# Kernel tuning notes

Measured on AMD Instinct MI355X. Metric: run time of the kernel, lower is better.

The kernel has to match this reference:

```python
import jax, jax.numpy as jnp
import numpy as np

DIMS = [1024, 2048, 2048, 51]
B, P = 16, 1024


def setup_inputs() -> dict:
    key = jax.random.key(0)
    ks = jax.random.split(key, 1 + 2 * (len(DIMS) - 1))
    inp = {
        "num_pairs": P,
        "classifier_input": jax.random.normal(ks[0], (B, P, DIMS[0]), dtype=jnp.float32),
        "num_batches": B,
    }
    # Linear params, PyTorch-style: W[out, in], b[out]
    for li in range(len(DIMS) - 1):
        fan_in = DIMS[li]
        bound = 1.0 / np.sqrt(fan_in)
        inp[f"W{li}"] = jax.random.uniform(ks[1 + 2 * li], (DIMS[li + 1], fan_in), minval=-bound, maxval=bound, dtype=jnp.float32)
        inp[f"b{li}"] = jax.random.uniform(ks[2 + 2 * li], (DIMS[li + 1],), minval=-bound, maxval=bound, dtype=jnp.float32)
    return inp


def reference(num_pairs, classifier_input, num_batches, W0, b0, W1, b1, W2, b2):
    # Batched MLP over all (num_batches * num_pairs) vectors at once.
    # Original loops per (b, i); math is identical. dropout p=0.0 -> identity.
    x = classifier_input  # [B, P, d_in]
    x = jax.nn.relu(jnp.einsum("bpd,hd->bph", x, W0) + b0)
    x = jax.nn.relu(jnp.einsum("bpd,hd->bph", x, W1) + b1)
    out = jnp.einsum("bpd,od->bpo", x, W2) + b2  # [B, P, n_classes]
    return out
```

## Files before the change

kernel.cpp:

```cpp
#include <hip/hip_runtime.h>
#include <hip/hip_bf16.h>
#include <stdint.h>

typedef __attribute__((ext_vector_type(8))) short short8;
typedef __attribute__((ext_vector_type(8))) uint16_t ushort8;
typedef __attribute__((ext_vector_type(4))) float floatx4;

#define TK 64


__device__ __forceinline__ uint16_t f2bf_bits(float f) {
    uint32_t u = __builtin_bit_cast(uint32_t, f);
    u += 0x7FFFu + ((u >> 16) & 1u);
    return (uint16_t)(u >> 16);
}

__device__ __forceinline__ void async_copy16(const void* g, void* l) {
    auto gp = (const __attribute__((address_space(1))) uint32_t*)(uintptr_t)g;
    auto lp = (__attribute__((address_space(3))) uint32_t*)(uint32_t)(uintptr_t)l;
    __builtin_amdgcn_global_load_lds(gp, lp, 16, 0, 0);
}

__device__ __forceinline__ void cvt8_one(const float* __restrict__ s, uint16_t* __restrict__ d) {
    floatx4 a = *(const floatx4*)(s);
    floatx4 b = *(const floatx4*)(s + 4);
    ushort8 o;
#pragma unroll
    for (int k = 0; k < 4; k++) { o[k] = f2bf_bits(a[k]); o[k + 4] = f2bf_bits(b[k]); }
    *(ushort8*)(d) = o;
}


__global__ void cvt8(const float* __restrict__ src, uint16_t* __restrict__ dst, int n) {
    int i = (blockIdx.x * 256 + threadIdx.x) * 8;
    if (i < n) cvt8_one(src + i, dst + i);
}

__global__ void cvt_weights(const float* __restrict__ W0, const float* __restrict__ W1,
                            const float* __restrict__ W2,
                            uint16_t* __restrict__ o0, uint16_t* __restrict__ o1,
                            uint16_t* __restrict__ o2) {
    int i = (blockIdx.x * 256 + threadIdx.x) * 8;
    if (i < 2097152) {
        cvt8_one(W0 + i, o0 + i);
    } else if (i < 2097152 + 4194304) {
        int j = i - 2097152;
        cvt8_one(W1 + j, o1 + j);
    } else {
        int j = i - 6291456;
        if (j < 131072) {
            int row = j >> 11;
            if (row < 51) cvt8_one(W2 + j, o2 + j);
            else { ushort8 z = {0,0,0,0,0,0,0,0}; *(ushort8*)(o2 + j) = z; }
        }
    }
}

__global__ void reduce_out(const float* __restrict__ part, const float* __restrict__ b2,
                           float* __restrict__ out, int M) {
    int idx = blockIdx.x * 256 + threadIdx.x;
    int o = idx & 63;
    if (o < 51) {
        int m = idx >> 6;
        float s = b2[o];
#pragma unroll
        for (int k = 0; k < 8; k++) s += part[(size_t)k * M * 64 + idx];
        out[m * 51 + o] = s;
    }
}


template <int MI, int NJ, int SPLITK, bool RELU, bool PARTIAL>
__global__ __launch_bounds__(256, 2)
void gemm_bt(const uint16_t* __restrict__ A,
             const uint16_t* __restrict__ W,
             const float* __restrict__ bias,
             void* __restrict__ out,
             int M, int N, int lda, int kspan, int ldc, int nstore)
{
    constexpr int TMv = MI * 32;
    constexpr int TNv = NJ * 32;
    constexpr int ACH = TMv / 32;
    constexpr int BCH = TNv / 32;

    __shared__ alignas(16) uint16_t sA[TMv * TK];
    __shared__ alignas(16) uint16_t sB[TNv * TK];

    const int tid  = threadIdx.x;
    const int wave = tid >> 6;
    const int lane = tid & 63;

    const int f = blockIdx.x;
    int m0, n0, kbeg;
    float* opart = (float*)out;
    if constexpr (SPLITK > 1) {
        const int kidx = f & (SPLITK - 1);
        kbeg = kidx * kspan;
        m0   = (f >> 3) * TMv;
        n0   = 0;
        opart += (size_t)kidx * M * ldc;
    } else {
        kbeg = 0;
        const int xcd = f & 7;
        const int loc = f >> 3;
        const int per = (int)gridDim.x >> 3;
        const int nt  = N / TNv;
        n0 = (loc % nt) * TNv;
        m0 = (xcd * (per / nt) + loc / nt) * TMv;
    }

    floatx4 acc[MI][NJ];
    const floatx4 zero = {0.f, 0.f, 0.f, 0.f};
#pragma unroll
    for (int i = 0; i < MI; i++)
#pragma unroll
        for (int j = 0; j < NJ; j++) acc[i][j] = zero;

    const int wr = (wave >> 1) * MI * 16;
    const int wc = (wave & 1) * NJ * 16;

    const int sr   = lane >> 3;
    const int scol = ((lane & 7) ^ sr) * 8;

    const uint16_t* ap[ACH];
    const uint16_t* bp[BCH];
#pragma unroll
    for (int t = 0; t < ACH; t++)
        ap[t] = A + (size_t)(m0 + (wave + 4 * t) * 8 + sr) * lda + kbeg + scol;
#pragma unroll
    for (int t = 0; t < BCH; t++)
        bp[t] = W + (size_t)(n0 + (wave + 4 * t) * 8 + sr) * lda + kbeg + scol;

    const int fm = lane & 15;
    const int fr = fm & 7;
    const int kgb = lane >> 4;

    const int niter = kspan / TK;
    for (int it = 0; it < niter; it++) {
#pragma unroll
        for (int t = 0; t < ACH; t++) {
            async_copy16(ap[t], sA + (wave + 4 * t) * 512);
            ap[t] += TK;
        }
#pragma unroll
        for (int t = 0; t < BCH; t++) {
            async_copy16(bp[t], sB + (wave + 4 * t) * 512);
            bp[t] += TK;
        }
        __syncthreads();

#pragma unroll
        for (int kk = 0; kk < 2; kk++) {
            const int slot = ((kgb + 4 * kk) ^ fr) * 8;
            short8 af[MI], bfr[NJ];
#pragma unroll
            for (int i = 0; i < MI; i++)
                af[i] = *(const short8*)(sA + (wr + i * 16 + fm) * TK + slot);
#pragma unroll
            for (int j = 0; j < NJ; j++)
                bfr[j] = *(const short8*)(sB + (wc + j * 16 + fm) * TK + slot);
#pragma unroll
            for (int i = 0; i < MI; i++)
#pragma unroll
                for (int j = 0; j < NJ; j++)
                    acc[i][j] = __builtin_amdgcn_mfma_f32_16x16x32_bf16(af[i], bfr[j], acc[i][j], 0, 0, 0);
        }
        __syncthreads();
    }

    const int cr = (lane >> 4) * 4;
    const int cc = lane & 15;
#pragma unroll
    for (int i = 0; i < MI; i++) {
        const int gmb = m0 + wr + i * 16 + cr;
#pragma unroll
        for (int j = 0; j < NJ; j++) {
            const int gn = n0 + wc + j * 16 + cc;
            if (gn < nstore) {
                float bv = 0.f;
                if constexpr (!PARTIAL) bv = bias[gn];
#pragma unroll
                for (int r = 0; r < 4; r++) {
                    float v = acc[i][j][r] + bv;
                    if (RELU) v = fmaxf(v, 0.f);
                    const size_t idx = (size_t)(gmb + r) * ldc + gn;
                    if constexpr (PARTIAL) opart[idx] = v;
                    else                   ((uint16_t*)out)[idx] = f2bf_bits(v);
                }
            }
        }
    }
}


extern "C" void kernel_launch(void* const* d_in, const int* in_sizes, int n_in,
                              void* d_out, int out_size, void* d_ws, size_t ws_size,
                              hipStream_t stream) {
    (void)in_sizes; (void)n_in; (void)out_size; (void)ws_size;
    const float* X  = (const float*)d_in[1];
    const float* W0 = (const float*)d_in[3];
    const float* b0 = (const float*)d_in[4];
    const float* W1 = (const float*)d_in[5];
    const float* b1 = (const float*)d_in[6];
    const float* W2 = (const float*)d_in[7];
    const float* b2 = (const float*)d_in[8];

    const int M = 16384;

    char* w = (char*)d_ws;
    uint16_t* X0  = (uint16_t*)w; w += (size_t)M * 1024 * 2;
    uint16_t* X1  = (uint16_t*)w; w += (size_t)M * 2048 * 2;
    uint16_t* X2  = (uint16_t*)w; w += (size_t)M * 2048 * 2;
    uint16_t* W0b = (uint16_t*)w; w += (size_t)2048 * 1024 * 2;
    uint16_t* W1b = (uint16_t*)w; w += (size_t)2048 * 2048 * 2;
    uint16_t* W2b = (uint16_t*)w; w += (size_t)64 * 2048 * 2;
    float* part = (float*)X0;

    cvt8<<<M * 1024 / 8 / 256, 256, 0, stream>>>(X, X0, M * 1024);
    cvt_weights<<<(2097152 + 4194304 + 131072) / 8 / 256, 256, 0, stream>>>(
        W0, W1, W2, W0b, W1b, W2b);

    gemm_bt<4, 8, 1, true, false><<<dim3((M / 128) * (2048 / 256)), 256, 0, stream>>>(
        X0, W0b, b0, X1, M, 2048, 1024, 1024, 2048, 2048);
    gemm_bt<4, 8, 1, true, false><<<dim3((M / 128) * (2048 / 256)), 256, 0, stream>>>(
        X1, W1b, b1, X2, M, 2048, 2048, 2048, 2048, 2048);
    gemm_bt<4, 2, 8, false, true><<<dim3((M / 128) * 8), 256, 0, stream>>>(
        X2, W2b, nullptr, part, M, 64, 2048, 256, 64, 64);
    reduce_out<<<M * 64 / 256, 256, 0, stream>>>(part, b2, (float*)d_out, M);
}
```

Measured before the change: 347.8 us.

## Pre-permute operands to fragment layout and load MFMA fragments directly from global

Conversion kernels now write activations and weights in a 16-row fragment-major layout so each lane's short8 MFMA operand is contiguous. The GEMM drops shared-memory staging and barriers, loading fragments straight into registers with a two-stage register prefetch. GEMM epilogues also write outputs in that permuted layout for the next layer. The tile shrinks to 128x128 with higher occupancy, giving up LDS-based reuse across waves in exchange for no LDS round-trip or synchronization, at the cost of more global/L2 traffic.

```diff
diff --git a/kernel.cpp b/kernel.cpp
--- a/kernel.cpp
+++ b/kernel.cpp
@@ -5,8 +5,6 @@
 typedef __attribute__((ext_vector_type(8))) short short8;
 typedef __attribute__((ext_vector_type(8))) uint16_t ushort8;
 typedef __attribute__((ext_vector_type(4))) float floatx4;
-
-#define TK 64
 
 
 __device__ __forceinline__ uint16_t f2bf_bits(float f) {
@@ -15,12 +13,6 @@
     return (uint16_t)(u >> 16);
 }
 
-__device__ __forceinline__ void async_copy16(const void* g, void* l) {
-    auto gp = (const __attribute__((address_space(1))) uint32_t*)(uintptr_t)g;
-    auto lp = (__attribute__((address_space(3))) uint32_t*)(uint32_t)(uintptr_t)l;
-    __builtin_amdgcn_global_load_lds(gp, lp, 16, 0, 0);
-}
-
 __device__ __forceinline__ void cvt8_one(const float* __restrict__ s, uint16_t* __restrict__ d) {
     floatx4 a = *(const floatx4*)(s);
     floatx4 b = *(const floatx4*)(s + 4);
@@ -30,28 +22,37 @@
     *(ushort8*)(d) = o;
 }
 
-
-__global__ void cvt8(const float* __restrict__ src, uint16_t* __restrict__ dst, int n) {
-    int i = (blockIdx.x * 256 + threadIdx.x) * 8;
-    if (i < n) cvt8_one(src + i, dst + i);
-}
-
-__global__ void cvt_weights(const float* __restrict__ W0, const float* __restrict__ W1,
-                            const float* __restrict__ W2,
-                            uint16_t* __restrict__ o0, uint16_t* __restrict__ o1,
-                            uint16_t* __restrict__ o2) {
-    int i = (blockIdx.x * 256 + threadIdx.x) * 8;
-    if (i < 2097152) {
-        cvt8_one(W0 + i, o0 + i);
-    } else if (i < 2097152 + 4194304) {
-        int j = i - 2097152;
-        cvt8_one(W1 + j, o1 + j);
+__device__ __forceinline__ size_t frag_off(int row, int kg , int K) {
+    return (size_t)(row >> 4) * 16 * K + ((size_t)kg * 16 + (row & 15)) * 8;
+}
+
+
+__global__ void cvt_x(const float* __restrict__ src, uint16_t* __restrict__ dst) {
+    int g = blockIdx.x * 256 + threadIdx.x;
+    int m  = g >> 7;
+    int kg = g & 127;
+    cvt8_one(src + (size_t)m * 1024 + kg * 8, dst + frag_off(m, kg, 1024));
+}
+
+__global__ void cvt_w(const float* __restrict__ W0, const float* __restrict__ W1,
+                      const float* __restrict__ W2,
+                      uint16_t* __restrict__ o0, uint16_t* __restrict__ o1,
+                      uint16_t* __restrict__ o2) {
+    int g = blockIdx.x * 256 + threadIdx.x;
+    if (g < 262144) {
+        int r = g >> 7, kg = g & 127;
+        cvt8_one(W0 + (size_t)r * 1024 + kg * 8, o0 + frag_off(r, kg, 1024));
+    } else if (g < 262144 + 524288) {
+        int j = g - 262144;
+        int r = j >> 8, kg = j & 255;
+        cvt8_one(W1 + (size_t)r * 2048 + kg * 8, o1 + frag_off(r, kg, 2048));
     } else {
-        int j = i - 6291456;
-        if (j < 131072) {
-            int row = j >> 11;
-            if (row < 51) cvt8_one(W2 + j, o2 + j);
-            else { ushort8 z = {0,0,0,0,0,0,0,0}; *(ushort8*)(o2 + j) = z; }
+        int j = g - 786432;
+        if (j < 16384) {
+            int r = j >> 8, kg = j & 255;
+            uint16_t* d = o2 + frag_off(r, kg, 2048);
+            if (r < 51) cvt8_one(W2 + (size_t)r * 2048 + kg * 8, d);
+            else { ushort8 z = {0,0,0,0,0,0,0,0}; *(ushort8*)d = z; }
         }
     }
 }
@@ -71,20 +72,15 @@
 
 
 template <int MI, int NJ, int SPLITK, bool RELU, bool PARTIAL>
-__global__ __launch_bounds__(256, 2)
-void gemm_bt(const uint16_t* __restrict__ A,
-             const uint16_t* __restrict__ W,
-             const float* __restrict__ bias,
-             void* __restrict__ out,
-             int M, int N, int lda, int kspan, int ldc, int nstore)
+__global__ __launch_bounds__(256, 3)
+void gemm_direct(const uint16_t* __restrict__ A,
+                 const uint16_t* __restrict__ W,
+                 const float* __restrict__ bias,
+                 void* __restrict__ out,
+                 int M, int N, int lda, int kspan, int ldc, int nstore)
 {
     constexpr int TMv = MI * 32;
     constexpr int TNv = NJ * 32;
-    constexpr int ACH = TMv / 32;
-    constexpr int BCH = TNv / 32;
-
-    __shared__ alignas(16) uint16_t sA[TMv * TK];
-    __shared__ alignas(16) uint16_t sB[TNv * TK];
 
     const int tid  = threadIdx.x;
     const int wave = tid >> 6;
@@ -109,6 +105,11 @@
         m0 = (xcd * (per / nt) + loc / nt) * TMv;
     }
 
+    const int wr = (wave >> 1) * MI * 16;
+    const int wc = (wave & 1) * NJ * 16;
+    const int pa0 = (m0 + wr) >> 4;
+    const int pb0 = (n0 + wc) >> 4;
+
     floatx4 acc[MI][NJ];
     const floatx4 zero = {0.f, 0.f, 0.f, 0.f};
 #pragma unroll
@@ -116,56 +117,37 @@
 #pragma unroll
         for (int j = 0; j < NJ; j++) acc[i][j] = zero;
 
-    const int wr = (wave >> 1) * MI * 16;
-    const int wc = (wave & 1) * NJ * 16;
-
-    const int sr   = lane >> 3;
-    const int scol = ((lane & 7) ^ sr) * 8;
-
-    const uint16_t* ap[ACH];
-    const uint16_t* bp[BCH];
-#pragma unroll
-    for (int t = 0; t < ACH; t++)
-        ap[t] = A + (size_t)(m0 + (wave + 4 * t) * 8 + sr) * lda + kbeg + scol;
-#pragma unroll
-    for (int t = 0; t < BCH; t++)
-        bp[t] = W + (size_t)(n0 + (wave + 4 * t) * 8 + sr) * lda + kbeg + scol;
-
-    const int fm = lane & 15;
-    const int fr = fm & 7;
-    const int kgb = lane >> 4;
-
-    const int niter = kspan / TK;
-    for (int it = 0; it < niter; it++) {
-#pragma unroll
-        for (int t = 0; t < ACH; t++) {
-            async_copy16(ap[t], sA + (wave + 4 * t) * 512);
-            ap[t] += TK;
-        }
-#pragma unroll
-        for (int t = 0; t < BCH; t++) {
-            async_copy16(bp[t], sB + (wave + 4 * t) * 512);
-            bp[t] += TK;
-        }
-        __syncthreads();
-
-#pragma unroll
-        for (int kk = 0; kk < 2; kk++) {
-            const int slot = ((kgb + 4 * kk) ^ fr) * 8;
-            short8 af[MI], bfr[NJ];
-#pragma unroll
-            for (int i = 0; i < MI; i++)
-                af[i] = *(const short8*)(sA + (wr + i * 16 + fm) * TK + slot);
+    const uint16_t* ap[MI];
+    const uint16_t* bp[NJ];
+#pragma unroll
+    for (int i = 0; i < MI; i++)
+        ap[i] = A + (size_t)(pa0 + i) * 16 * lda + (size_t)kbeg * 16 + lane * 8;
+#pragma unroll
+    for (int j = 0; j < NJ; j++)
+        bp[j] = W + (size_t)(pb0 + j) * 16 * lda + (size_t)kbeg * 16 + lane * 8;
+
+    auto loadfr = [&](short8 (&fa)[MI], short8 (&fb)[NJ]) {
+#pragma unroll
+        for (int i = 0; i < MI; i++) { fa[i] = *(const short8*)ap[i]; ap[i] += 512; }
+#pragma unroll
+        for (int j = 0; j < NJ; j++) { fb[j] = *(const short8*)bp[j]; bp[j] += 512; }
+    };
+    auto domfma = [&](short8 (&fa)[MI], short8 (&fb)[NJ]) {
+#pragma unroll
+        for (int i = 0; i < MI; i++)
 #pragma unroll
             for (int j = 0; j < NJ; j++)
-                bfr[j] = *(const short8*)(sB + (wc + j * 16 + fm) * TK + slot);
-#pragma unroll
-            for (int i = 0; i < MI; i++)
-#pragma unroll
-                for (int j = 0; j < NJ; j++)
-                    acc[i][j] = __builtin_amdgcn_mfma_f32_16x16x32_bf16(af[i], bfr[j], acc[i][j], 0, 0, 0);
-        }
-        __syncthreads();
+                acc[i][j] = __builtin_amdgcn_mfma_f32_16x16x32_bf16(fa[i], fb[j], acc[i][j], 0, 0, 0);
+    };
+
+    short8 ca[MI], cb[NJ], na[MI], nb[NJ];
+    loadfr(ca, cb);
+    const int nit = kspan / 32;
+    for (int it = 0; it < nit; it += 2) {
+        loadfr(na, nb);
+        domfma(ca, cb);
+        if (it + 2 < nit) loadfr(ca, cb);
+        domfma(na, nb);
     }
 
     const int cr = (lane >> 4) * 4;
@@ -183,9 +165,13 @@
                 for (int r = 0; r < 4; r++) {
                     float v = acc[i][j][r] + bv;
                     if (RELU) v = fmaxf(v, 0.f);
-                    const size_t idx = (size_t)(gmb + r) * ldc + gn;
-                    if constexpr (PARTIAL) opart[idx] = v;
-                    else                   ((uint16_t*)out)[idx] = f2bf_bits(v);
+                    if constexpr (PARTIAL) {
+                        opart[(size_t)(gmb + r) * ldc + gn] = v;
+                    } else {
+                        const size_t idx = (size_t)(pa0 + i) * 16 * ldc +
+                                           ((size_t)(gn >> 3) * 16 + cr + r) * 8 + (gn & 7);
+                        ((uint16_t*)out)[idx] = f2bf_bits(v);
+                    }
                 }
             }
         }
@@ -216,15 +202,15 @@
     uint16_t* W2b = (uint16_t*)w; w += (size_t)64 * 2048 * 2;
     float* part = (float*)X0;
 
-    cvt8<<<M * 1024 / 8 / 256, 256, 0, stream>>>(X, X0, M * 1024);
-    cvt_weights<<<(2097152 + 4194304 + 131072) / 8 / 256, 256, 0, stream>>>(
+    cvt_x<<<M * 128 / 256, 256, 0, stream>>>(X, X0);
+    cvt_w<<<(262144 + 524288 + 16384) / 256, 256, 0, stream>>>(
         W0, W1, W2, W0b, W1b, W2b);
 
-    gemm_bt<4, 8, 1, true, false><<<dim3((M / 128) * (2048 / 256)), 256, 0, stream>>>(
+    gemm_direct<4, 4, 1, true, false><<<dim3((M / 128) * (2048 / 128)), 256, 0, stream>>>(
         X0, W0b, b0, X1, M, 2048, 1024, 1024, 2048, 2048);
-    gemm_bt<4, 8, 1, true, false><<<dim3((M / 128) * (2048 / 256)), 256, 0, stream>>>(
+    gemm_direct<4, 4, 1, true, false><<<dim3((M / 128) * (2048 / 128)), 256, 0, stream>>>(
         X1, W1b, b1, X2, M, 2048, 2048, 2048, 2048, 2048);
-    gemm_bt<4, 2, 8, false, true><<<dim3((M / 128) * 8), 256, 0, stream>>>(
+    gemm_direct<4, 2, 8, false, true><<<dim3((M / 128) * 8), 256, 0, stream>>>(
         X2, W2b, nullptr, part, M, 64, 2048, 256, 64, 64);
     reduce_out<<<M * 64 / 256, 256, 0, stream>>>(part, b2, (float*)d_out, M);
 }
```

Result: slower. 420.3 us (+20.8%).

## Fuse whole MLP pipeline into one cooperative persistent kernel with grid syncs

Applied to the files above, without the earlier changes.

Replaces the six separate launches (input/weight conversion, three GEMMs, reduction) with a single cooperative kernel of 512 persistent blocks. Each block loops over its share of tiles per stage, and grid.sync separates the stages. The aim is to remove launch gaps and per-launch tail overhead between stages. In exchange it adds grid-wide barriers and a fixed-size grid, and it requires co-residency of 512 blocks; if the cooperative launch fails, the code falls back to separate kernels.

```diff
diff --git a/kernel.cpp b/kernel.cpp
--- a/kernel.cpp
+++ b/kernel.cpp
@@ -1,12 +1,19 @@
 #include <hip/hip_runtime.h>
 #include <hip/hip_bf16.h>
+#include <hip/hip_cooperative_groups.h>
 #include <stdint.h>
+
+namespace cg = cooperative_groups;
 
 typedef __attribute__((ext_vector_type(8))) short short8;
 typedef __attribute__((ext_vector_type(8))) uint16_t ushort8;
 typedef __attribute__((ext_vector_type(4))) float floatx4;
 
 #define TK 64
+#define GRID_BLKS 512
+#define GRID_THREADS (GRID_BLKS * 256)
+#define MDIM 16384
+#define NCVT 2899968
 
 
 __device__ __forceinline__ uint16_t f2bf_bits(float f) {
@@ -30,67 +37,60 @@
     *(ushort8*)(d) = o;
 }
 
-
-__global__ void cvt8(const float* __restrict__ src, uint16_t* __restrict__ dst, int n) {
-    int i = (blockIdx.x * 256 + threadIdx.x) * 8;
-    if (i < n) cvt8_one(src + i, dst + i);
-}
-
-__global__ void cvt_weights(const float* __restrict__ W0, const float* __restrict__ W1,
-                            const float* __restrict__ W2,
-                            uint16_t* __restrict__ o0, uint16_t* __restrict__ o1,
-                            uint16_t* __restrict__ o2) {
-    int i = (blockIdx.x * 256 + threadIdx.x) * 8;
+__device__ __forceinline__ void cvt_item(
+    int i, const float* __restrict__ X,
+    const float* __restrict__ W0, const float* __restrict__ W1,
+    const float* __restrict__ W2,
+    uint16_t* __restrict__ X0, uint16_t* __restrict__ W0b,
+    uint16_t* __restrict__ W1b, uint16_t* __restrict__ W2b)
+{
     if (i < 2097152) {
-        cvt8_one(W0 + i, o0 + i);
-    } else if (i < 2097152 + 4194304) {
-        int j = i - 2097152;
-        cvt8_one(W1 + j, o1 + j);
+        cvt8_one(X + (size_t)i * 8, X0 + (size_t)i * 8);
+    } else if (i < 2097152 + 262144) {
+        const size_t j = (size_t)(i - 2097152) * 8;
+        cvt8_one(W0 + j, W0b + j);
+    } else if (i < 2097152 + 262144 + 524288) {
+        const size_t j = (size_t)(i - 2097152 - 262144) * 8;
+        cvt8_one(W1 + j, W1b + j);
     } else {
-        int j = i - 6291456;
-        if (j < 131072) {
-            int row = j >> 11;
-            if (row < 51) cvt8_one(W2 + j, o2 + j);
-            else { ushort8 z = {0,0,0,0,0,0,0,0}; *(ushort8*)(o2 + j) = z; }
-        }
-    }
-}
-
-__global__ void reduce_out(const float* __restrict__ part, const float* __restrict__ b2,
-                           float* __restrict__ out, int M) {
-    int idx = blockIdx.x * 256 + threadIdx.x;
-    int o = idx & 63;
+        const size_t j = (size_t)(i - NCVT + 16384) * 8;
+        const int row = (int)(j >> 11);
+        if (row < 51) cvt8_one(W2 + j, W2b + j);
+        else { ushort8 z = {0,0,0,0,0,0,0,0}; *(ushort8*)(W2b + j) = z; }
+    }
+}
+
+__device__ __forceinline__ void reduce_item(
+    int idx, const float* __restrict__ part, const float* __restrict__ b2,
+    float* __restrict__ out)
+{
+    const int o = idx & 63;
     if (o < 51) {
-        int m = idx >> 6;
+        const int m = idx >> 6;
         float s = b2[o];
 #pragma unroll
-        for (int k = 0; k < 8; k++) s += part[(size_t)k * M * 64 + idx];
+        for (int k = 0; k < 8; k++) s += part[(size_t)k * MDIM * 64 + idx];
         out[m * 51 + o] = s;
     }
 }
 
 
 template <int MI, int NJ, int SPLITK, bool RELU, bool PARTIAL>
-__global__ __launch_bounds__(256, 2)
-void gemm_bt(const uint16_t* __restrict__ A,
-             const uint16_t* __restrict__ W,
-             const float* __restrict__ bias,
-             void* __restrict__ out,
-             int M, int N, int lda, int kspan, int ldc, int nstore)
+__device__ __forceinline__ void gemm_tile(
+    uint16_t* __restrict__ sA, uint16_t* __restrict__ sB,
+    const uint16_t* __restrict__ A, const uint16_t* __restrict__ W,
+    const float* __restrict__ bias, void* __restrict__ out,
+    int f, int totf, int M, int N, int lda, int kspan, int ldc, int nstore)
 {
     constexpr int TMv = MI * 32;
     constexpr int TNv = NJ * 32;
     constexpr int ACH = TMv / 32;
     constexpr int BCH = TNv / 32;
 
-    __shared__ alignas(16) uint16_t sA[TMv * TK];
-    __shared__ alignas(16) uint16_t sB[TNv * TK];
-
     const int tid  = threadIdx.x;
     const int wave = tid >> 6;
     const int lane = tid & 63;
 
-    const int f = blockIdx.x;
     int m0, n0, kbeg;
     float* opart = (float*)out;
     if constexpr (SPLITK > 1) {
@@ -103,7 +103,7 @@
         kbeg = 0;
         const int xcd = f & 7;
         const int loc = f >> 3;
-        const int per = (int)gridDim.x >> 3;
+        const int per = totf >> 3;
         const int nt  = N / TNv;
         n0 = (loc % nt) * TNv;
         m0 = (xcd * (per / nt) + loc / nt) * TMv;
@@ -190,6 +190,86 @@
             }
         }
     }
+}
+
+
+__global__ __launch_bounds__(256, 2)
+void fused_mlp(const float* __restrict__ X,
+               const float* __restrict__ W0, const float* __restrict__ b0,
+               const float* __restrict__ W1, const float* __restrict__ b1,
+               const float* __restrict__ W2, const float* __restrict__ b2,
+               float* __restrict__ out,
+               uint16_t* __restrict__ X0, uint16_t* __restrict__ X1,
+               uint16_t* __restrict__ X2,
+               uint16_t* __restrict__ W0b, uint16_t* __restrict__ W1b,
+               uint16_t* __restrict__ W2b, float* __restrict__ part)
+{
+    __shared__ alignas(16) uint16_t sA[128 * TK];
+    __shared__ alignas(16) uint16_t sB[256 * TK];
+    cg::grid_group grid = cg::this_grid();
+
+    const int b    = blockIdx.x;
+    const int gtid = b * 256 + threadIdx.x;
+
+    for (int i = gtid; i < NCVT; i += GRID_THREADS)
+        cvt_item(i, X, W0, W1, W2, X0, W0b, W1b, W2b);
+    __threadfence();
+    grid.sync();
+
+#pragma unroll
+    for (int s = 0; s < 2; s++)
+        gemm_tile<4, 8, 1, true, false>(sA, sB, X0, W0b, b0, X1,
+                                        b + s * GRID_BLKS, 1024,
+                                        MDIM, 2048, 1024, 1024, 2048, 2048);
+    __threadfence();
+    grid.sync();
+
+#pragma unroll
+    for (int s = 0; s < 2; s++)
+        gemm_tile<4, 8, 1, true, false>(sA, sB, X1, W1b, b1, X2,
+                                        b + s * GRID_BLKS, 1024,
+                                        MDIM, 2048, 2048, 2048, 2048, 2048);
+    __threadfence();
+    grid.sync();
+
+#pragma unroll
+    for (int s = 0; s < 2; s++)
+        gemm_tile<4, 2, 8, false, true>(sA, sB, X2, W2b, nullptr, part,
+                                        b + s * GRID_BLKS, 1024,
+                                        MDIM, 64, 2048, 256, 64, 64);
+    __threadfence();
+    grid.sync();
+
+    for (int idx = gtid; idx < MDIM * 64; idx += GRID_THREADS)
+        reduce_item(idx, part, b2, out);
+}
+
+
+__global__ void k_cvt(const float* __restrict__ X,
+                      const float* __restrict__ W0, const float* __restrict__ W1,
+                      const float* __restrict__ W2,
+                      uint16_t* __restrict__ X0, uint16_t* __restrict__ W0b,
+                      uint16_t* __restrict__ W1b, uint16_t* __restrict__ W2b) {
+    int i = blockIdx.x * 256 + threadIdx.x;
+    if (i < NCVT) cvt_item(i, X, W0, W1, W2, X0, W0b, W1b, W2b);
+}
+
+template <int MI, int NJ, int SPLITK, bool RELU, bool PARTIAL>
+__global__ __launch_bounds__(256, 2)
+void k_gemm(const uint16_t* __restrict__ A, const uint16_t* __restrict__ W,
+            const float* __restrict__ bias, void* __restrict__ out,
+            int M, int N, int lda, int kspan, int ldc, int nstore) {
+    __shared__ alignas(16) uint16_t sA[MI * 32 * TK];
+    __shared__ alignas(16) uint16_t sB[NJ * 32 * TK];
+    gemm_tile<MI, NJ, SPLITK, RELU, PARTIAL>(sA, sB, A, W, bias, out,
+                                             blockIdx.x, (int)gridDim.x,
+                                             M, N, lda, kspan, ldc, nstore);
+}
+
+__global__ void k_reduce(const float* __restrict__ part, const float* __restrict__ b2,
+                         float* __restrict__ out) {
+    int idx = blockIdx.x * 256 + threadIdx.x;
+    if (idx < MDIM * 64) reduce_item(idx, part, b2, out);
 }
 
 
@@ -204,27 +284,31 @@
     const float* b1 = (const float*)d_in[6];
     const float* W2 = (const float*)d_in[7];
     const float* b2 = (const float*)d_in[8];
-
-    const int M = 16384;
+    float* outp = (float*)d_out;
 
     char* w = (char*)d_ws;
-    uint16_t* X0  = (uint16_t*)w; w += (size_t)M * 1024 * 2;
-    uint16_t* X1  = (uint16_t*)w; w += (size_t)M * 2048 * 2;
-    uint16_t* X2  = (uint16_t*)w; w += (size_t)M * 2048 * 2;
+    uint16_t* X0  = (uint16_t*)w; w += (size_t)MDIM * 1024 * 2;
+    uint16_t* X1  = (uint16_t*)w; w += (size_t)MDIM * 2048 * 2;
+    uint16_t* X2  = (uint16_t*)w; w += (size_t)MDIM * 2048 * 2;
     uint16_t* W0b = (uint16_t*)w; w += (size_t)2048 * 1024 * 2;
     uint16_t* W1b = (uint16_t*)w; w += (size_t)2048 * 2048 * 2;
     uint16_t* W2b = (uint16_t*)w; w += (size_t)64 * 2048 * 2;
     float* part = (float*)X0;
 
-    cvt8<<<M * 1024 / 8 / 256, 256, 0, stream>>>(X, X0, M * 1024);
-    cvt_weights<<<(2097152 + 4194304 + 131072) / 8 / 256, 256, 0, stream>>>(
-        W0, W1, W2, W0b, W1b, W2b);
-
-    gemm_bt<4, 8, 1, true, false><<<dim3((M / 128) * (2048 / 256)), 256, 0, stream>>>(
-        X0, W0b, b0, X1, M, 2048, 1024, 1024, 2048, 2048);
-    gemm_bt<4, 8, 1, true, false><<<dim3((M / 128) * (2048 / 256)), 256, 0, stream>>>(
-        X1, W1b, b1, X2, M, 2048, 2048, 2048, 2048, 2048);
-    gemm_bt<4, 2, 8, false, true><<<dim3((M / 128) * 8), 256, 0, stream>>>(
-        X2, W2b, nullptr, part, M, 64, 2048, 256, 64, 64);
-    reduce_out<<<M * 64 / 256, 256, 0, stream>>>(part, b2, (float*)d_out, M);
-}
+    void* args[] = { (void*)&X, (void*)&W0, (void*)&b0, (void*)&W1, (void*)&b1,
+                     (void*)&W2, (void*)&b2, (void*)&outp,
+                     (void*)&X0, (void*)&X1, (void*)&X2,
+                     (void*)&W0b, (void*)&W1b, (void*)&W2b, (void*)&part };
+    hipError_t err = hipLaunchCooperativeKernel((void*)fused_mlp, dim3(GRID_BLKS),
+                                                dim3(256), args, 0, stream);
+    if (err != hipSuccess) {
+        k_cvt<<<(NCVT + 255) / 256, 256, 0, stream>>>(X, W0, W1, W2, X0, W0b, W1b, W2b);
+        k_gemm<4, 8, 1, true, false><<<dim3(1024), 256, 0, stream>>>(
+            X0, W0b, b0, X1, MDIM, 2048, 1024, 1024, 2048, 2048);
+        k_gemm<4, 8, 1, true, false><<<dim3(1024), 256, 0, stream>>>(
+            X1, W1b, b1, X2, MDIM, 2048, 2048, 2048, 2048, 2048);
+        k_gemm<4, 2, 8, false, true><<<dim3(1024), 256, 0, stream>>>(
+            X2, W2b, nullptr, part, MDIM, 64, 2048, 256, 64, 64);
+        k_reduce<<<MDIM * 64 / 256, 256, 0, stream>>>(part, b2, outp);
+    }
+}
```

Measured after the change: 862.8 us. 148% more time.
